# Optimization experiments

Measured on AMD Instinct MI355X. Metric: run time of the kernel, lower is better.

Reference implementation:

```python
import jax, jax.numpy as jnp
import numpy as np

MD_S = 1
MD_R = 16
EVAL_STEPS = 7
INV_T = 100.0
EPS = 1e-6

B, C, S = 16, 512, 4096  # batch, channels, flattened spatial


def setup_inputs() -> dict:
    key = jax.random.key(0)
    k1, k2 = jax.random.split(key)
    x = jax.random.uniform(k1, (B, C, S), dtype=jnp.float32)  # non-negative input for NMF
    bases = jax.random.uniform(k2, (B * MD_S, S, MD_R), dtype=jnp.float32)
    # F.normalize(bases, dim=1)
    bases = bases / (jnp.linalg.norm(bases, axis=1, keepdims=True) + 1e-12)
    return {"x": x, "bases": bases}


def _nmf_step(xm, bases, coef):
    # xm: (BS, D, N), bases: (BS, D, R), coef: (BS, N, R)
    # multiplicative update for coef
    num = jnp.einsum('bdn,bdr->bnr', xm, bases)
    den = jnp.einsum('bnr,brs->bns', coef, jnp.einsum('bdr,bds->brs', bases, bases))
    coef = coef * num / (den + EPS)
    # multiplicative update for bases
    num = jnp.einsum('bdn,bnr->bdr', xm, coef)
    den = jnp.einsum('bdr,brs->bds', bases, jnp.einsum('bnr,bns->brs', coef, coef))
    bases = bases * num / (den + EPS)
    return bases, coef


def _local_inference(xm, bases):
    # coef init: softmax(inv_t * x^T bases)
    coef = jax.nn.softmax(INV_T * jnp.einsum('bdn,bdr->bnr', xm, bases), axis=-1)

    def body(carry, _):
        b, c = _nmf_step(xm, carry[0], carry[1])
        return (b, c), None

    (bases, coef), _ = jax.lax.scan(body, (bases, coef), None, length=EVAL_STEPS)
    return bases, coef


def reference(x, bases):
    Bb, Cc, Ss = x.shape
    D = Ss
    N = Cc // MD_S
    xm = x.reshape(Bb * MD_S, N, D).transpose(0, 2, 1)  # (BS, D, N)

    bases_i, coef_i = jax.lax.stop_gradient(_local_inference(xm, bases))

    # compute_coef (differentiable in the original module)
    num = jnp.einsum('bdn,bdr->bnr', xm, bases_i)
    den = jnp.einsum('bnr,brs->bns', coef_i, jnp.einsum('bdr,bds->brs', bases_i, bases_i))
    coef = coef_i * num / (den + EPS)

    # x_rec = bases @ coef^T -> (BS, D, N) -> transpose -> (B, C, S)
    out = jnp.einsum('bdr,bnr->bdn', bases_i, coef)
    out = out.transpose(0, 2, 1).reshape(Bb, Cc, Ss)
    return out
```

## Files before the change

kernel.cpp:

```cpp
#include <hip/hip_runtime.h>

#define EPS 1e-6f

template <int CTRL>
__device__ __forceinline__ float dpp_add(float v) {
  int moved = __builtin_amdgcn_update_dpp(0, __float_as_int(v), CTRL, 0xF, 0xF, false);
  return v + __int_as_float(moved);
}

__global__ __launch_bounds__(256) void kernelA(
    const float* __restrict__ x, const float* __restrict__ bases,
    float* __restrict__ P, float* __restrict__ coef,
    float* __restrict__ CtC, int do_softmax)
{
  __shared__ __align__(16) float lb[512 * 20];
  const int tid = threadIdx.x;
  if (blockIdx.x < 16) CtC[blockIdx.x * 256 + tid] = 0.0f;
  const int b = blockIdx.x >> 4;
  const int grp = blockIdx.x & 15;
  const int w = tid >> 6;
  const int lane = tid & 63;
  const int n0 = grp * 32 + w * 8;
  const float* __restrict__ xp = x + ((size_t)(b * 512 + n0)) * 4096;
  const float* __restrict__ bp = bases + ((size_t)b) * 4096 * 16;

  float acc[8][16];
#pragma unroll
  for (int i = 0; i < 8; ++i)
#pragma unroll
    for (int r = 0; r < 16; ++r) acc[i][r] = 0.0f;

  for (int c = 0; c < 8; ++c) {
    const int d0 = c * 512;
    const float4* __restrict__ src = (const float4*)(bp + (size_t)d0 * 16);
#pragma unroll
    for (int k = 0; k < 8; ++k) {
      int idx = k * 256 + tid;
      int dl = idx >> 2, q = idx & 3;
      *(float4*)(&lb[dl * 20 + q * 4]) = src[idx];
    }
    __syncthreads();
#pragma unroll
    for (int j = 0; j < 8; ++j) {
      const int dl = j * 64 + lane;
      float xv[8];
#pragma unroll
      for (int i = 0; i < 8; ++i) xv[i] = xp[(size_t)i * 4096 + d0 + dl];
      const float* row = &lb[dl * 20];
#pragma unroll
      for (int q = 0; q < 4; ++q) {
        float4 bv = *(const float4*)(row + q * 4);
#pragma unroll
        for (int i = 0; i < 8; ++i) {
          acc[i][q * 4 + 0] = fmaf(xv[i], bv.x, acc[i][q * 4 + 0]);
          acc[i][q * 4 + 1] = fmaf(xv[i], bv.y, acc[i][q * 4 + 1]);
          acc[i][q * 4 + 2] = fmaf(xv[i], bv.z, acc[i][q * 4 + 2]);
          acc[i][q * 4 + 3] = fmaf(xv[i], bv.w, acc[i][q * 4 + 3]);
        }
      }
    }
    __syncthreads();
  }

#pragma unroll
  for (int i = 0; i < 8; ++i)
#pragma unroll
    for (int r = 0; r < 16; ++r) {
      float v = acc[i][r];
      v = dpp_add<0x121>(v);
      v = dpp_add<0x122>(v);
      v = dpp_add<0x124>(v);
      v = dpp_add<0x128>(v);
      v += __shfl_xor(v, 16, 64);
      v += __shfl_xor(v, 32, 64);
      acc[i][r] = v;
    }

  if (lane == 0) {
    float* __restrict__ prow = P + ((size_t)(b * 512 + n0)) * 16;
#pragma unroll
    for (int i = 0; i < 8; ++i)
#pragma unroll
      for (int r = 0; r < 16; ++r) prow[i * 16 + r] = acc[i][r];
    if (do_softmax) {
      float* __restrict__ crow = coef + ((size_t)(b * 512 + n0)) * 16;
#pragma unroll
      for (int i = 0; i < 8; ++i) {
        float m = acc[i][0];
#pragma unroll
        for (int r = 1; r < 16; ++r) m = fmaxf(m, acc[i][r]);
        float e[16];
        float s = 0.0f;
#pragma unroll
        for (int r = 0; r < 16; ++r) { e[r] = __expf(100.0f * (acc[i][r] - m)); s += e[r]; }
        float inv = 1.0f / s;
#pragma unroll
        for (int r = 0; r < 16; ++r) crow[i * 16 + r] = e[r] * inv;
      }
    }
  }
}

__global__ __launch_bounds__(256) void kernelGram(
    const float* __restrict__ M, float* __restrict__ out, int L)
{
  __shared__ __align__(16) float sm[256 * 20];
  __shared__ __align__(16) float part[4 * 272];
  const int tid = threadIdx.x;
  const int b = blockIdx.y;
  const int sl = blockIdx.x;
  const float4* __restrict__ src = (const float4*)(M + ((size_t)b * L + (size_t)sl * 256) * 16);
#pragma unroll
  for (int k = 0; k < 4; ++k) {
    int idx = k * 256 + tid;
    int row = idx >> 2, q = idx & 3;
    *(float4*)(&sm[row * 20 + q * 4]) = src[idx];
  }
  __syncthreads();
  const int rq = tid & 3;
  const int s = (tid >> 2) & 15;
  const int g = tid >> 6;
  float a0 = 0.f, a1 = 0.f, a2 = 0.f, a3 = 0.f;
#pragma unroll 4
  for (int l = g * 64; l < g * 64 + 64; ++l) {
    float4 bv = *(const float4*)(&sm[l * 20 + rq * 4]);
    float cs = sm[l * 20 + s];
    a0 = fmaf(cs, bv.x, a0);
    a1 = fmaf(cs, bv.y, a1);
    a2 = fmaf(cs, bv.z, a2);
    a3 = fmaf(cs, bv.w, a3);
  }
  *(float4*)(&part[g * 272 + s * 16 + rq * 4]) = make_float4(a0, a1, a2, a3);
  __syncthreads();
  float v = part[0 * 272 + tid] + part[1 * 272 + tid] + part[2 * 272 + tid] + part[3 * 272 + tid];
  atomicAdd(out + b * 256 + tid, v);
}

__global__ __launch_bounds__(256) void kernelCU(
    float* __restrict__ coef, const float* __restrict__ P,
    const float* __restrict__ BtBr, float* __restrict__ BtBz)
{
  const int tid = threadIdx.x;
  BtBz[blockIdx.x * 128 + (tid & 127)] = 0.0f;
  const int b = blockIdx.x >> 1;
  const int n = ((blockIdx.x & 1) << 8) + tid;
  float* __restrict__ crow = coef + ((size_t)(b * 512 + n)) * 16;
  const float* __restrict__ prow = P + ((size_t)(b * 512 + n)) * 16;
  const float* __restrict__ btb = BtBr + b * 256;
  float cv[16], den[16];
#pragma unroll
  for (int r = 0; r < 16; ++r) cv[r] = crow[r];
#pragma unroll
  for (int r = 0; r < 16; ++r) den[r] = 0.f;
#pragma unroll
  for (int s2 = 0; s2 < 16; ++s2) {
    const float bs = cv[s2];
#pragma unroll
    for (int r = 0; r < 16; ++r) den[r] = fmaf(bs, btb[s2 * 16 + r], den[r]);
  }
#pragma unroll
  for (int r = 0; r < 16; ++r) crow[r] = cv[r] * prow[r] / (den[r] + EPS);
}

__global__ __launch_bounds__(256) void kernelB(
    const float* __restrict__ x, const float* __restrict__ coef,
    float* __restrict__ bases, const float* __restrict__ CtC)
{
  const int tid = threadIdx.x;
  const int b = blockIdx.y;
  const int d = blockIdx.x * 256 + tid;
  const float* __restrict__ xp = x + ((size_t)b * 512) * 4096 + d;
  const float* __restrict__ cp = coef + (size_t)b * 512 * 16;
  float acc[16];
#pragma unroll
  for (int r = 0; r < 16; ++r) acc[r] = 0.f;
#pragma unroll 4
  for (int n = 0; n < 512; ++n) {
    const float xv = xp[(size_t)n * 4096];
    const float* __restrict__ crow = cp + n * 16;
#pragma unroll
    for (int r = 0; r < 16; ++r) acc[r] = fmaf(xv, crow[r], acc[r]);
  }
  float* __restrict__ brow = bases + ((size_t)b * 4096 + d) * 16;
  float bv[16];
#pragma unroll
  for (int r = 0; r < 16; ++r) bv[r] = brow[r];
  const float* __restrict__ ctc = CtC + b * 256;
  float den[16];
#pragma unroll
  for (int r = 0; r < 16; ++r) den[r] = 0.f;
#pragma unroll
  for (int s2 = 0; s2 < 16; ++s2) {
    const float bs = bv[s2];
#pragma unroll
    for (int r = 0; r < 16; ++r) den[r] = fmaf(bs, ctc[s2 * 16 + r], den[r]);
  }
#pragma unroll
  for (int r = 0; r < 16; ++r) brow[r] = bv[r] * acc[r] / (den[r] + EPS);
}

__global__ __launch_bounds__(256) void kernelOut(
    const float* __restrict__ bases, const float* __restrict__ coef,
    float* __restrict__ out)
{
  const int tid = threadIdx.x;
  const int b = blockIdx.y;
  const int d = blockIdx.x * 256 + tid;
  const float* __restrict__ brow = bases + ((size_t)b * 4096 + d) * 16;
  float bv[16];
#pragma unroll
  for (int r = 0; r < 16; ++r) bv[r] = brow[r];
  const float* __restrict__ cp = coef + (size_t)b * 512 * 16;
  float* __restrict__ op = out + ((size_t)b * 512) * 4096 + d;
#pragma unroll 4
  for (int n = 0; n < 512; ++n) {
    const float* __restrict__ crow = cp + n * 16;
    float v = 0.f;
#pragma unroll
    for (int r = 0; r < 16; ++r) v = fmaf(bv[r], crow[r], v);
    op[(size_t)n * 4096] = v;
  }
}

extern "C" void kernel_launch(void* const* d_in, const int* in_sizes, int n_in,
                              void* d_out, int out_size, void* d_ws, size_t ws_size,
                              hipStream_t stream) {
  const float* x = (const float*)d_in[0];
  const float* bases_in = (const float*)d_in[1];
  float* out = (float*)d_out;
  float* ws = (float*)d_ws;

  float* bases = ws;
  float* coef  = bases + 1048576;
  float* P     = coef + 131072;
  float* btb0  = P + 131072;
  float* btb1  = btb0 + 4096;
  float* ctc   = btb1 + 4096;
  float* btb[2] = {btb0, btb1};

  hipMemsetAsync(btb0, 0, 4096 * sizeof(float), stream);
  hipMemcpyAsync(bases, bases_in, 1048576 * sizeof(float),
                 hipMemcpyDeviceToDevice, stream);

  kernelA<<<256, 256, 0, stream>>>(x, bases, P, coef, ctc, 1);
  kernelGram<<<dim3(16, 16), 256, 0, stream>>>(bases, btb0, 4096);

  for (int t = 0; t < 7; ++t) {
    if (t > 0) kernelA<<<256, 256, 0, stream>>>(x, bases, P, coef, ctc, 0);
    kernelCU<<<32, 256, 0, stream>>>(coef, P, btb[t & 1], btb[(t + 1) & 1]);
    kernelGram<<<dim3(2, 16), 256, 0, stream>>>(coef, ctc, 512);
    kernelB<<<dim3(16, 16), 256, 0, stream>>>(x, coef, bases, ctc);
    kernelGram<<<dim3(16, 16), 256, 0, stream>>>(bases, btb[(t + 1) & 1], 4096);
  }

  kernelA<<<256, 256, 0, stream>>>(x, bases, P, coef, ctc, 0);
  kernelCU<<<32, 256, 0, stream>>>(coef, P, btb[1], btb[0]);
  kernelOut<<<dim3(16, 16), 256, 0, stream>>>(bases, coef, out);
}
```

Baseline: 1.083 ms.

## Fuse Gram updates into producers, split-N kernelB, widen kernelA and kernelOut

kernelA now runs 512 threads per block and splits the D reduction across two halves, combining the partial results in shared memory. The coef and bases Gram computations are fused into kernelCU and a new kernelBfin, which removes two kernel launches per iteration. kernelB is split into a partial-sum kernel over four N slices plus a finalize pass, raising the block count to fill more CUs at the cost of extra global traffic. kernelOut is re-tiled to compute four d values per thread with float4 stores and more blocks.

```diff
diff --git a/kernel.cpp b/kernel.cpp
--- a/kernel.cpp
+++ b/kernel.cpp
@@ -8,21 +8,23 @@
   return v + __int_as_float(moved);
 }
 
-__global__ __launch_bounds__(256) void kernelA(
+__global__ __launch_bounds__(512) void kernelA(
     const float* __restrict__ x, const float* __restrict__ bases,
     float* __restrict__ P, float* __restrict__ coef,
     float* __restrict__ CtC, int do_softmax)
 {
-  __shared__ __align__(16) float lb[512 * 20];
-  const int tid = threadIdx.x;
-  if (blockIdx.x < 16) CtC[blockIdx.x * 256 + tid] = 0.0f;
+  __shared__ __align__(16) float lb[20480];
+  const int tid = threadIdx.x;
+  if (blockIdx.x < 16 && tid < 256) CtC[blockIdx.x * 256 + tid] = 0.0f;
   const int b = blockIdx.x >> 4;
   const int grp = blockIdx.x & 15;
   const int w = tid >> 6;
   const int lane = tid & 63;
-  const int n0 = grp * 32 + w * 8;
-  const float* __restrict__ xp = x + ((size_t)(b * 512 + n0)) * 4096;
-  const float* __restrict__ bp = bases + ((size_t)b) * 4096 * 16;
+  const int h = w >> 2;
+  const int rg = w & 3;
+  const int n0 = grp * 32 + rg * 8;
+  const float* __restrict__ xp = x + ((size_t)(b * 512 + n0)) * 4096 + h * 2048;
+  const float4* __restrict__ srcf4 = (const float4*)(bases + ((size_t)b) * 4096 * 16);
 
   float acc[8][16];
 #pragma unroll
@@ -30,23 +32,26 @@
 #pragma unroll
     for (int r = 0; r < 16; ++r) acc[i][r] = 0.0f;
 
-  for (int c = 0; c < 8; ++c) {
-    const int d0 = c * 512;
-    const float4* __restrict__ src = (const float4*)(bp + (size_t)d0 * 16);
+  for (int c = 0; c < 4; ++c) {
 #pragma unroll
     for (int k = 0; k < 8; ++k) {
-      int idx = k * 256 + tid;
-      int dl = idx >> 2, q = idx & 3;
-      *(float4*)(&lb[dl * 20 + q * 4]) = src[idx];
+      int idx = k * 512 + tid;
+      int buf = idx >> 11;
+      int rem = idx & 2047;
+      int dl = rem >> 2, q = rem & 3;
+      int cg = c + buf * 4;
+      *(float4*)(&lb[buf * 10240 + dl * 20 + q * 4]) = srcf4[(cg * 512 + dl) * 4 + q];
     }
     __syncthreads();
+    const float* __restrict__ lbh = lb + h * 10240;
+    const float* __restrict__ xpc = xp + c * 512;
 #pragma unroll
     for (int j = 0; j < 8; ++j) {
       const int dl = j * 64 + lane;
       float xv[8];
 #pragma unroll
-      for (int i = 0; i < 8; ++i) xv[i] = xp[(size_t)i * 4096 + d0 + dl];
-      const float* row = &lb[dl * 20];
+      for (int i = 0; i < 8; ++i) xv[i] = xpc[(size_t)i * 4096 + dl];
+      const float* row = &lbh[dl * 20];
 #pragma unroll
       for (int q = 0; q < 4; ++q) {
         float4 bv = *(const float4*)(row + q * 4);
@@ -77,25 +82,34 @@
     }
 
   if (lane == 0) {
-    float* __restrict__ prow = P + ((size_t)(b * 512 + n0)) * 16;
 #pragma unroll
     for (int i = 0; i < 8; ++i)
 #pragma unroll
-      for (int r = 0; r < 16; ++r) prow[i * 16 + r] = acc[i][r];
+      for (int r = 0; r < 16; ++r) lb[(h * 4 + rg) * 128 + i * 16 + r] = acc[i][r];
+  }
+  __syncthreads();
+  {
+    const int row = tid >> 4;
+    const int r = tid & 15;
+    const int prg = row >> 3, pi = row & 7;
+    float p = lb[(prg)*128 + pi * 16 + r] + lb[(4 + prg) * 128 + pi * 16 + r];
+    P[((size_t)(b * 512 + grp * 32 + row)) * 16 + r] = p;
     if (do_softmax) {
-      float* __restrict__ crow = coef + ((size_t)(b * 512 + n0)) * 16;
-#pragma unroll
-      for (int i = 0; i < 8; ++i) {
-        float m = acc[i][0];
-#pragma unroll
-        for (int r = 1; r < 16; ++r) m = fmaxf(m, acc[i][r]);
+      lb[1024 + tid] = p;
+      __syncthreads();
+      if (tid < 32) {
+        const float* pf = &lb[1024 + tid * 16];
+        float m = pf[0];
+#pragma unroll
+        for (int rr = 1; rr < 16; ++rr) m = fmaxf(m, pf[rr]);
         float e[16];
         float s = 0.0f;
 #pragma unroll
-        for (int r = 0; r < 16; ++r) { e[r] = __expf(100.0f * (acc[i][r] - m)); s += e[r]; }
+        for (int rr = 0; rr < 16; ++rr) { e[rr] = __expf(100.0f * (pf[rr] - m)); s += e[rr]; }
         float inv = 1.0f / s;
-#pragma unroll
-        for (int r = 0; r < 16; ++r) crow[i * 16 + r] = e[r] * inv;
+        float* __restrict__ crow = coef + ((size_t)(b * 512 + grp * 32 + tid)) * 16;
+#pragma unroll
+        for (int rr = 0; rr < 16; ++rr) crow[rr] = e[rr] * inv;
       }
     }
   }
@@ -138,8 +152,10 @@
 
 __global__ __launch_bounds__(256) void kernelCU(
     float* __restrict__ coef, const float* __restrict__ P,
-    const float* __restrict__ BtBr, float* __restrict__ BtBz)
-{
+    const float* __restrict__ BtBr, float* __restrict__ BtBz,
+    float* __restrict__ CtCadd)
+{
+  __shared__ __align__(16) float sm[256 * 20 + 4 * 272];
   const int tid = threadIdx.x;
   BtBz[blockIdx.x * 128 + (tid & 127)] = 0.0f;
   const int b = blockIdx.x >> 1;
@@ -159,29 +175,78 @@
     for (int r = 0; r < 16; ++r) den[r] = fmaf(bs, btb[s2 * 16 + r], den[r]);
   }
 #pragma unroll
-  for (int r = 0; r < 16; ++r) crow[r] = cv[r] * prow[r] / (den[r] + EPS);
-}
-
-__global__ __launch_bounds__(256) void kernelB(
+  for (int r = 0; r < 16; ++r) {
+    float cn = cv[r] * prow[r] / (den[r] + EPS);
+    crow[r] = cn;
+    sm[tid * 20 + r] = cn;
+  }
+  __syncthreads();
+  const int rq = tid & 3;
+  const int s = (tid >> 2) & 15;
+  const int g = tid >> 6;
+  float a0 = 0.f, a1 = 0.f, a2 = 0.f, a3 = 0.f;
+#pragma unroll 4
+  for (int l = g * 64; l < g * 64 + 64; ++l) {
+    float4 bv = *(const float4*)(&sm[l * 20 + rq * 4]);
+    float cs = sm[l * 20 + s];
+    a0 = fmaf(cs, bv.x, a0);
+    a1 = fmaf(cs, bv.y, a1);
+    a2 = fmaf(cs, bv.z, a2);
+    a3 = fmaf(cs, bv.w, a3);
+  }
+  float* part = sm + 5120;
+  *(float4*)(&part[g * 272 + s * 16 + rq * 4]) = make_float4(a0, a1, a2, a3);
+  __syncthreads();
+  float v = part[0 * 272 + tid] + part[1 * 272 + tid] + part[2 * 272 + tid] + part[3 * 272 + tid];
+  atomicAdd(CtCadd + b * 256 + tid, v);
+}
+
+__global__ __launch_bounds__(256) void kernelBacc(
     const float* __restrict__ x, const float* __restrict__ coef,
-    float* __restrict__ bases, const float* __restrict__ CtC)
-{
-  const int tid = threadIdx.x;
-  const int b = blockIdx.y;
-  const int d = blockIdx.x * 256 + tid;
-  const float* __restrict__ xp = x + ((size_t)b * 512) * 4096 + d;
-  const float* __restrict__ cp = coef + (size_t)b * 512 * 16;
+    float* __restrict__ qpart)
+{
+  const int tid = threadIdx.x;
+  const int dt = blockIdx.x, ns = blockIdx.y, b = blockIdx.z;
+  const int d = dt * 256 + tid;
+  const float* __restrict__ xp = x + ((size_t)(b * 512 + ns * 128)) * 4096 + d;
+  const float* __restrict__ cp = coef + ((size_t)(b * 512 + ns * 128)) * 16;
   float acc[16];
 #pragma unroll
   for (int r = 0; r < 16; ++r) acc[r] = 0.f;
 #pragma unroll 4
-  for (int n = 0; n < 512; ++n) {
+  for (int n = 0; n < 128; ++n) {
     const float xv = xp[(size_t)n * 4096];
     const float* __restrict__ crow = cp + n * 16;
 #pragma unroll
     for (int r = 0; r < 16; ++r) acc[r] = fmaf(xv, crow[r], acc[r]);
   }
-  float* __restrict__ brow = bases + ((size_t)b * 4096 + d) * 16;
+  float* __restrict__ qp = qpart + (((size_t)(ns * 16 + b)) * 4096 + d) * 16;
+#pragma unroll
+  for (int q = 0; q < 4; ++q)
+    *(float4*)(qp + q * 4) = make_float4(acc[q * 4], acc[q * 4 + 1], acc[q * 4 + 2], acc[q * 4 + 3]);
+}
+
+__global__ __launch_bounds__(256) void kernelBfin(
+    const float* __restrict__ qpart, float* __restrict__ bases,
+    const float* __restrict__ CtC, float* __restrict__ BtBadd)
+{
+  __shared__ __align__(16) float sm[256 * 20 + 4 * 272];
+  const int tid = threadIdx.x;
+  const int dt = blockIdx.x, b = blockIdx.y;
+  const int d = dt * 256 + tid;
+  float acc[16];
+#pragma unroll
+  for (int r = 0; r < 16; ++r) acc[r] = 0.f;
+#pragma unroll
+  for (int ns = 0; ns < 4; ++ns) {
+    const float* __restrict__ qp = qpart + (((size_t)(ns * 16 + b)) * 4096 + d) * 16;
+#pragma unroll
+    for (int q = 0; q < 4; ++q) {
+      float4 v = *(const float4*)(qp + q * 4);
+      acc[q * 4 + 0] += v.x; acc[q * 4 + 1] += v.y; acc[q * 4 + 2] += v.z; acc[q * 4 + 3] += v.w;
+    }
+  }
+  float* __restrict__ brow = bases + ((size_t)(b * 4096 + d)) * 16;
   float bv[16];
 #pragma unroll
   for (int r = 0; r < 16; ++r) bv[r] = brow[r];
@@ -196,7 +261,30 @@
     for (int r = 0; r < 16; ++r) den[r] = fmaf(bs, ctc[s2 * 16 + r], den[r]);
   }
 #pragma unroll
-  for (int r = 0; r < 16; ++r) brow[r] = bv[r] * acc[r] / (den[r] + EPS);
+  for (int r = 0; r < 16; ++r) {
+    float bn = bv[r] * acc[r] / (den[r] + EPS);
+    brow[r] = bn;
+    sm[tid * 20 + r] = bn;
+  }
+  __syncthreads();
+  const int rq = tid & 3;
+  const int s = (tid >> 2) & 15;
+  const int g = tid >> 6;
+  float a0 = 0.f, a1 = 0.f, a2 = 0.f, a3 = 0.f;
+#pragma unroll 4
+  for (int l = g * 64; l < g * 64 + 64; ++l) {
+    float4 bq = *(const float4*)(&sm[l * 20 + rq * 4]);
+    float cs = sm[l * 20 + s];
+    a0 = fmaf(cs, bq.x, a0);
+    a1 = fmaf(cs, bq.y, a1);
+    a2 = fmaf(cs, bq.z, a2);
+    a3 = fmaf(cs, bq.w, a3);
+  }
+  float* part = sm + 5120;
+  *(float4*)(&part[g * 272 + s * 16 + rq * 4]) = make_float4(a0, a1, a2, a3);
+  __syncthreads();
+  float v = part[0 * 272 + tid] + part[1 * 272 + tid] + part[2 * 272 + tid] + part[3 * 272 + tid];
+  atomicAdd(BtBadd + b * 256 + tid, v);
 }
 
 __global__ __launch_bounds__(256) void kernelOut(
@@ -204,21 +292,29 @@
     float* __restrict__ out)
 {
   const int tid = threadIdx.x;
-  const int b = blockIdx.y;
-  const int d = blockIdx.x * 256 + tid;
-  const float* __restrict__ brow = bases + ((size_t)b * 4096 + d) * 16;
-  float bv[16];
-#pragma unroll
-  for (int r = 0; r < 16; ++r) bv[r] = brow[r];
-  const float* __restrict__ cp = coef + (size_t)b * 512 * 16;
-  float* __restrict__ op = out + ((size_t)b * 512) * 4096 + d;
-#pragma unroll 4
-  for (int n = 0; n < 512; ++n) {
+  const int dt = blockIdx.x, ns = blockIdx.y, b = blockIdx.z;
+  const int d0 = dt * 1024 + tid * 4;
+  float bv[4][16];
+#pragma unroll
+  for (int k = 0; k < 4; ++k) {
+    const float* __restrict__ brow = bases + ((size_t)(b * 4096 + d0 + k)) * 16;
+#pragma unroll
+    for (int r = 0; r < 16; ++r) bv[k][r] = brow[r];
+  }
+  const float* __restrict__ cp = coef + ((size_t)(b * 512 + ns * 32)) * 16;
+  float* __restrict__ op = out + ((size_t)(b * 512 + ns * 32)) * 4096 + d0;
+#pragma unroll 4
+  for (int n = 0; n < 32; ++n) {
     const float* __restrict__ crow = cp + n * 16;
-    float v = 0.f;
-#pragma unroll
-    for (int r = 0; r < 16; ++r) v = fmaf(bv[r], crow[r], v);
-    op[(size_t)n * 4096] = v;
+    float v[4];
+#pragma unroll
+    for (int k = 0; k < 4; ++k) {
+      float s = 0.f;
+#pragma unroll
+      for (int r = 0; r < 16; ++r) s = fmaf(bv[k][r], crow[r], s);
+      v[k] = s;
+    }
+    *(float4*)(op + (size_t)n * 4096) = make_float4(v[0], v[1], v[2], v[3]);
   }
 }
 
@@ -236,24 +332,24 @@
   float* btb0  = P + 131072;
   float* btb1  = btb0 + 4096;
   float* ctc   = btb1 + 4096;
+  float* qpart = ctc + 4096;
   float* btb[2] = {btb0, btb1};
 
   hipMemsetAsync(btb0, 0, 4096 * sizeof(float), stream);
   hipMemcpyAsync(bases, bases_in, 1048576 * sizeof(float),
                  hipMemcpyDeviceToDevice, stream);
 
-  kernelA<<<256, 256, 0, stream>>>(x, bases, P, coef, ctc, 1);
+  kernelA<<<256, 512, 0, stream>>>(x, bases, P, coef, ctc, 1);
   kernelGram<<<dim3(16, 16), 256, 0, stream>>>(bases, btb0, 4096);
 
   for (int t = 0; t < 7; ++t) {
-    if (t > 0) kernelA<<<256, 256, 0, stream>>>(x, bases, P, coef, ctc, 0);
-    kernelCU<<<32, 256, 0, stream>>>(coef, P, btb[t & 1], btb[(t + 1) & 1]);
-    kernelGram<<<dim3(2, 16), 256, 0, stream>>>(coef, ctc, 512);
-    kernelB<<<dim3(16, 16), 256, 0, stream>>>(x, coef, bases, ctc);
-    kernelGram<<<dim3(16, 16), 256, 0, stream>>>(bases, btb[(t + 1) & 1], 4096);
-  }
-
-  kernelA<<<256, 256, 0, stream>>>(x, bases, P, coef, ctc, 0);
-  kernelCU<<<32, 256, 0, stream>>>(coef, P, btb[1], btb[0]);
-  kernelOut<<<dim3(16, 16), 256, 0, stream>>>(bases, coef, out);
-}
+    if (t > 0) kernelA<<<256, 512, 0, stream>>>(x, bases, P, coef, ctc, 0);
+    kernelCU<<<32, 256, 0, stream>>>(coef, P, btb[t & 1], btb[(t + 1) & 1], ctc);
+    kernelBacc<<<dim3(16, 4, 16), 256, 0, stream>>>(x, coef, qpart);
+    kernelBfin<<<dim3(16, 16), 256, 0, stream>>>(qpart, bases, ctc, btb[(t + 1) & 1]);
+  }
+
+  kernelA<<<256, 512, 0, stream>>>(x, bases, P, coef, ctc, 0);
+  kernelCU<<<32, 256, 0, stream>>>(coef, P, btb[1], btb[0], ctc);
+  kernelOut<<<dim3(4, 16, 16), 256, 0, stream>>>(bases, coef, out);
+}
```

Result: no change. 1.101 ms (+1.7%).
